# Optimization experiments

Hardware: AMD Instinct MI355X
Metric: run time of the kernel (lower is better)

The kernel has to match this reference:

```python
import jax, jax.numpy as jnp
import numpy as np

D_MODEL = 1024
H = 16
HEAD_DIM = D_MODEL // H  # 64


def setup_inputs() -> dict:
    key = jax.random.key(0)
    ks = jax.random.split(key, 11)
    B, S, D = 1, 4096, D_MODEL
    scale = 1.0 / np.sqrt(D)
    inp = {
        'q': jax.random.normal(ks[0], (B, S, D), jnp.float32),
        'k': jax.random.normal(ks[1], (B, S, D), jnp.float32),
        'v': jax.random.normal(ks[2], (B, S, D), jnp.float32),
        'w_q': jax.random.normal(ks[3], (D, D), jnp.float32) * scale,
        'b_q': jnp.zeros((D,), jnp.float32),
        'w_k': jax.random.normal(ks[4], (D, D), jnp.float32) * scale,
        'b_k': jnp.zeros((D,), jnp.float32),
        'w_v': jax.random.normal(ks[5], (D, D), jnp.float32) * scale,
        'b_v': jnp.zeros((D,), jnp.float32),
        'w_o': jax.random.normal(ks[6], (D, D), jnp.float32) * scale,
        'b_o': jnp.zeros((D,), jnp.float32),
    }
    return inp


def reference(q, k, v, w_q, b_q, w_k, b_k, w_v, b_v, w_o, b_o):
    B, Sq, D = q.shape
    Sk = k.shape[1]
    # Linear projections (torch Linear: x @ W.T + b), split into heads: [B,H,S,hd]
    Q = (q @ w_q.T + b_q).reshape(B, Sq, H, HEAD_DIM).transpose(0, 2, 1, 3)
    K = (k @ w_k.T + b_k).reshape(B, Sk, H, HEAD_DIM).transpose(0, 2, 1, 3)
    V = (v @ w_v.T + b_v).reshape(B, Sk, H, HEAD_DIM).transpose(0, 2, 1, 3)
    # Naive attention: full [B,H,Sq,Sk] scores, softmax, then AV
    scores = jnp.einsum('bhqd,bhkd->bhqk', Q, K) / jnp.sqrt(jnp.float32(HEAD_DIM))
    attn = jax.nn.softmax(scores, axis=-1)
    ctx = jnp.einsum('bhqk,bhkd->bhqd', attn, V)
    concat = ctx.transpose(0, 2, 1, 3).reshape(B, Sq, D)
    return concat @ w_o.T + b_o
```

## Files before the change

kernel.cpp:

```cpp
#include <hip/hip_runtime.h>
#include <stdint.h>

#define S_LEN 4096
#define DM 1024
#define NH 16

typedef __attribute__((ext_vector_type(8))) short short8;
typedef __attribute__((ext_vector_type(4))) float float4v;
typedef __attribute__((ext_vector_type(4))) unsigned short ushort4v;

typedef __attribute__((address_space(1))) const void* as1cvp;
typedef __attribute__((address_space(3))) void* as3vp;

#define MFMA16(a, b, c) __builtin_amdgcn_mfma_f32_16x16x32_bf16((a), (b), (c), 0, 0, 0)
#define GLOAD_LDS16(g, l) \
  __builtin_amdgcn_global_load_lds((as1cvp)(g), (as3vp)(l), 16, 0, 0)

__device__ __forceinline__ unsigned short f2bf(float f) {
  unsigned u = __float_as_uint(f);
  u += 0x7fffu + ((u >> 16) & 1u);
  return (unsigned short)(u >> 16);
}

__global__ __launch_bounds__(256) void cast_all(
    const float* __restrict__ q, const float* __restrict__ k, const float* __restrict__ v,
    const float* __restrict__ wq, const float* __restrict__ wk, const float* __restrict__ wv,
    const float* __restrict__ wo, unsigned short* __restrict__ dst)
{
  const float* src; size_t off; int n;
  switch (blockIdx.y) {
    case 0: src = q;  off = 0u;        n = 4194304; break;
    case 1: src = k;  off = 4194304u;  n = 4194304; break;
    case 2: src = v;  off = 8388608u;  n = 4194304; break;
    case 3: src = wq; off = 12582912u; n = 1048576; break;
    case 4: src = wk; off = 13631488u; n = 1048576; break;
    case 5: src = wv; off = 14680064u; n = 1048576; break;
    default: src = wo; off = 15728640u; n = 1048576; break;
  }
  int nv = n >> 2;
  for (int i = blockIdx.x * blockDim.x + threadIdx.x; i < nv; i += gridDim.x * blockDim.x) {
    float4v val = ((const float4v*)src)[i];
    ushort4v o;
    o.x = f2bf(val.x); o.y = f2bf(val.y); o.z = f2bf(val.z); o.w = f2bf(val.w);
    ((ushort4v*)(dst + off))[i] = o;
  }
}

template<int MODE>
__device__ __forceinline__ void gemm128(
    const unsigned short* __restrict__ A, const unsigned short* __restrict__ Bw,
    unsigned short* Cb, float* Cf, const float* __restrict__ bias, float alpha,
    unsigned short* As, unsigned short* Bs)
{
  const int K = 1024, N = 1024;
  int bm = blockIdx.x, bn = blockIdx.y;
  int t = threadIdx.x, lane = t & 63, w = t >> 6;
  int l15 = lane & 15, l4 = lane >> 4;
  int wr = w >> 1, wc = w & 1;

  float4v acc[4][4] = {};

  for (int kt = 0; kt < K / 32; ++kt) {
#pragma unroll
    for (int i = 0; i < 2; ++i) {
      int ci = i * 256 + t;
      int r = ci >> 2, cb = ci & 3;
      GLOAD_LDS16(A + (size_t)(bm * 128 + r) * K + kt * 32 + cb * 8,
                  As + (size_t)(i * 256 + w * 64) * 8);
      GLOAD_LDS16(Bw + (size_t)(bn * 128 + r) * K + kt * 32 + cb * 8,
                  Bs + (size_t)(i * 256 + w * 64) * 8);
    }
    __syncthreads();
    short8 af[4], bfr[4];
#pragma unroll
    for (int mf = 0; mf < 4; ++mf)
      af[mf] = *(const short8*)&As[(wr * 64 + mf * 16 + l15) * 32 + l4 * 8];
#pragma unroll
    for (int nf = 0; nf < 4; ++nf)
      bfr[nf] = *(const short8*)&Bs[(wc * 64 + nf * 16 + l15) * 32 + l4 * 8];
#pragma unroll
    for (int mf = 0; mf < 4; ++mf)
#pragma unroll
      for (int nf = 0; nf < 4; ++nf)
        acc[mf][nf] = MFMA16(af[mf], bfr[nf], acc[mf][nf]);
    __syncthreads();
  }

#pragma unroll
  for (int mf = 0; mf < 4; ++mf)
#pragma unroll
    for (int nf = 0; nf < 4; ++nf) {
      int col = bn * 128 + wc * 64 + nf * 16 + l15;
      float bv = bias[col];
#pragma unroll
      for (int j = 0; j < 4; ++j) {
        int row = bm * 128 + wr * 64 + mf * 16 + l4 * 4 + j;
        float val = (acc[mf][nf][j] + bv) * alpha;
        if (MODE == 1)      Cf[(size_t)row * N + col] = val;
        else if (MODE == 2) Cb[(size_t)col * S_LEN + row] = f2bf(val);
        else                Cb[(size_t)row * N + col] = f2bf(val);
      }
    }
}

__global__ __launch_bounds__(256) void proj_qkv(
    const unsigned short* xq, const unsigned short* xk, const unsigned short* xv,
    const unsigned short* wq, const unsigned short* wk, const unsigned short* wv,
    unsigned short* Qp, unsigned short* Kp, unsigned short* Vt,
    const float* bq, const float* bk, const float* bv)
{
  __shared__ unsigned short As[128 * 32], Bs[128 * 32];
  switch (blockIdx.z) {
    case 0:  gemm128<0>(xq, wq, Qp, nullptr, bq, 0.125f, As, Bs); break;
    case 1:  gemm128<0>(xk, wk, Kp, nullptr, bk, 1.0f,   As, Bs); break;
    default: gemm128<2>(xv, wv, Vt, nullptr, bv, 1.0f,   As, Bs); break;
  }
}

__global__ __launch_bounds__(256) void proj_o(
    const unsigned short* ctx, const unsigned short* wo, float* out, const float* bo)
{
  __shared__ unsigned short As[128 * 32], Bs[128 * 32];
  gemm128<1>(ctx, wo, nullptr, out, bo, 1.0f, As, Bs);
}

template<int BUF>
__device__ __forceinline__ void attn_tile(
    int kt,
    const unsigned short* kb0, const unsigned short* kb1,
    const unsigned short* vb0, const unsigned short* vb1,
    unsigned short* pw, const unsigned short* pr,
    const unsigned short* kg, const unsigned short* vg,
    unsigned short* kls, unsigned short* vls,
    const short8 (&qf)[2][2], float4v (&acc_o)[2][4],
    float (&m_run)[2], float (&l_run)[2], int l4)
{
  if (kt + 1 < 64) {
    GLOAD_LDS16(kg + (size_t)(kt + 1) * (64 * DM),            kls + (1 - BUF) * 4096);
    GLOAD_LDS16(kg + (size_t)(kt + 1) * (64 * DM) + 32 * DM,  kls + (1 - BUF) * 4096 + 2048);
    GLOAD_LDS16(vg + (kt + 1) * 64,                           vls + (1 - BUF) * 4096);
    GLOAD_LDS16(vg + (kt + 1) * 64 + 32 * S_LEN,              vls + (1 - BUF) * 4096 + 2048);
  }

  float4v sc[2][4];
#pragma unroll
  for (int nf = 0; nf < 4; ++nf) {
    short8 kf0 = *(const short8*)(kb0 + BUF * 4096 + nf * 1024);
    short8 kf1 = *(const short8*)(kb1 + BUF * 4096 + nf * 1024);
#pragma unroll
    for (int mf = 0; mf < 2; ++mf) {
      float4v z = {0.f, 0.f, 0.f, 0.f};
      z = MFMA16(kf0, qf[mf][0], z);
      sc[mf][nf] = MFMA16(kf1, qf[mf][1], z);
    }
  }

#pragma unroll
  for (int mf = 0; mf < 2; ++mf) {
    float mx = fmaxf(fmaxf(fmaxf(sc[mf][0][0], sc[mf][0][1]), sc[mf][0][2]), sc[mf][0][3]);
#pragma unroll
    for (int nf = 1; nf < 4; ++nf)
      mx = fmaxf(fmaxf(fmaxf(fmaxf(mx, sc[mf][nf][0]), sc[mf][nf][1]), sc[mf][nf][2]), sc[mf][nf][3]);
    mx = fmaxf(mx, __shfl_xor(mx, 16));
    mx = fmaxf(mx, __shfl_xor(mx, 32));

    if (!__all(mx <= m_run[mf] + 8.f)) {
      float mnew = fmaxf(m_run[mf], mx);
      float corr = __expf(m_run[mf] - mnew);
      m_run[mf] = mnew;
      l_run[mf] *= corr;
#pragma unroll
      for (int j = 0; j < 4; ++j) {
        float cj = __shfl(corr, l4 * 4 + j);
#pragma unroll
        for (int nf2 = 0; nf2 < 4; ++nf2) acc_o[mf][nf2][j] *= cj;
      }
    }

    float ps = 0.f;
#pragma unroll
    for (int nf = 0; nf < 4; ++nf) {
      float p0 = __expf(sc[mf][nf][0] - m_run[mf]);
      float p1 = __expf(sc[mf][nf][1] - m_run[mf]);
      float p2 = __expf(sc[mf][nf][2] - m_run[mf]);
      float p3 = __expf(sc[mf][nf][3] - m_run[mf]);
      ps += (p0 + p1) + (p2 + p3);
      unsigned lo, hi;
      asm("v_cvt_pk_bf16_f32 %0, %1, %2" : "=v"(lo) : "v"(p0), "v"(p1));
      asm("v_cvt_pk_bf16_f32 %0, %1, %2" : "=v"(hi) : "v"(p2), "v"(p3));
      uint2 u; u.x = lo; u.y = hi;
      *(uint2*)(pw + mf * 1152 + nf * 16) = u;
    }
    ps += __shfl_xor(ps, 16);
    ps += __shfl_xor(ps, 32);
    l_run[mf] += ps;
  }

  short8 pf[2][2];
#pragma unroll
  for (int mf = 0; mf < 2; ++mf)
#pragma unroll
    for (int kc = 0; kc < 2; ++kc)
      pf[mf][kc] = *(const short8*)(pr + mf * 1152 + kc * 32);

#pragma unroll
  for (int nfd = 0; nfd < 4; ++nfd) {
    short8 vf0 = *(const short8*)(vb0 + BUF * 4096 + nfd * 1024);
    short8 vf1 = *(const short8*)(vb1 + BUF * 4096 + nfd * 1024);
#pragma unroll
    for (int mf = 0; mf < 2; ++mf) {
      acc_o[mf][nfd] = MFMA16(pf[mf][0], vf0, acc_o[mf][nfd]);
      acc_o[mf][nfd] = MFMA16(pf[mf][1], vf1, acc_o[mf][nfd]);
    }
  }
  __syncthreads();
}

__global__ __launch_bounds__(256) void attn_fused(
    const unsigned short* __restrict__ Qp, const unsigned short* __restrict__ Kp,
    const unsigned short* __restrict__ Vt, unsigned short* __restrict__ ctx)
{
  __shared__ unsigned short Ks[2][64 * 64];
  __shared__ unsigned short Vts[2][64 * 64];
  __shared__ unsigned short Ps[4][32 * 72];

  int bid = blockIdx.x;
  int wg = (bid & 7) * 64 + (bid >> 3);
  int h = wg >> 5, qt = wg & 31;

  int t = threadIdx.x, lane = t & 63, w = t >> 6;
  int l15 = lane & 15, l4 = lane >> 4;

  short8 qf[2][2];
  int qrow0 = qt * 128 + w * 32;
#pragma unroll
  for (int mf = 0; mf < 2; ++mf)
#pragma unroll
    for (int ks = 0; ks < 2; ++ks)
      qf[mf][ks] = *(const short8*)&Qp[(size_t)(qrow0 + mf * 16 + l15) * DM + h * 64 + ks * 32 + l4 * 8];

  float4v acc_o[2][4] = {};
  float m_run[2] = {-INFINITY, -INFINITY};
  float l_run[2] = {0.f, 0.f};

  const int swz = l15 & 7;
  const unsigned short* kb0 = &Ks[0][l15 * 64 + ((l4) ^ swz) * 8];
  const unsigned short* kb1 = &Ks[0][l15 * 64 + ((4 + l4) ^ swz) * 8];
  const unsigned short* vb0 = &Vts[0][l15 * 64 + ((l4) ^ swz) * 8];
  const unsigned short* vb1 = &Vts[0][l15 * 64 + ((4 + l4) ^ swz) * 8];
  unsigned short* pw = &Ps[w][l15 * 72 + l4 * 4];
  const unsigned short* pr = &Ps[w][l15 * 72 + l4 * 8];

  int sr = t >> 3, sp = t & 7;
  int slb = sp ^ (sr & 7);
  const unsigned short* kg = Kp + (size_t)sr * DM + h * 64 + slb * 8;
  const unsigned short* vg = Vt + (size_t)(h * 64 + sr) * S_LEN + slb * 8;
  unsigned short* kls = &Ks[0][t * 8];
  unsigned short* vls = &Vts[0][t * 8];

  GLOAD_LDS16(kg,                kls);
  GLOAD_LDS16(kg + 32 * DM,      kls + 2048);
  GLOAD_LDS16(vg,                vls);
  GLOAD_LDS16(vg + 32 * S_LEN,   vls + 2048);
  __syncthreads();

  for (int kt = 0; kt < 64; kt += 2) {
    attn_tile<0>(kt,     kb0, kb1, vb0, vb1, pw, pr, kg, vg, kls, vls, qf, acc_o, m_run, l_run, l4);
    attn_tile<1>(kt + 1, kb0, kb1, vb0, vb1, pw, pr, kg, vg, kls, vls, qf, acc_o, m_run, l_run, l4);
  }

#pragma unroll
  for (int mf = 0; mf < 2; ++mf) {
#pragma unroll
    for (int j = 0; j < 4; ++j) {
      float lj = __shfl(l_run[mf], l4 * 4 + j);
      float inv = 1.0f / lj;
#pragma unroll
      for (int nfd = 0; nfd < 4; ++nfd) {
        int row = qrow0 + mf * 16 + l4 * 4 + j;
        int col = h * 64 + nfd * 16 + l15;
        ctx[(size_t)row * DM + col] = f2bf(acc_o[mf][nfd][j] * inv);
      }
    }
  }
}

extern "C" void kernel_launch(void* const* d_in, const int* in_sizes, int n_in,
                              void* d_out, int out_size, void* d_ws, size_t ws_size,
                              hipStream_t stream) {
  const float* q  = (const float*)d_in[0];
  const float* k  = (const float*)d_in[1];
  const float* v  = (const float*)d_in[2];
  const float* wq = (const float*)d_in[3];
  const float* bq = (const float*)d_in[4];
  const float* wk = (const float*)d_in[5];
  const float* bk = (const float*)d_in[6];
  const float* wv = (const float*)d_in[7];
  const float* bv = (const float*)d_in[8];
  const float* wo = (const float*)d_in[9];
  const float* bo = (const float*)d_in[10];

  unsigned short* ws  = (unsigned short*)d_ws;
  unsigned short* qb  = ws;
  unsigned short* kb  = ws + 4194304u;
  unsigned short* vb  = ws + 8388608u;
  unsigned short* wqb = ws + 12582912u;
  unsigned short* wkb = ws + 13631488u;
  unsigned short* wvb = ws + 14680064u;
  unsigned short* wob = ws + 15728640u;
  unsigned short* Qp  = ws + 16777216u;
  unsigned short* Kp  = ws + 20971520u;
  unsigned short* Vt  = ws + 25165824u;
  unsigned short* ctx = qb;
  float* out = (float*)d_out;

  cast_all<<<dim3(1024, 7), 256, 0, stream>>>(q, k, v, wq, wk, wv, wo, ws);
  proj_qkv<<<dim3(32, 8, 3), 256, 0, stream>>>(qb, kb, vb, wqb, wkb, wvb, Qp, Kp, Vt, bq, bk, bv);
  attn_fused<<<dim3(512), 256, 0, stream>>>(Qp, Kp, Vt, ctx);
  proj_o<<<dim3(32, 8), 256, 0, stream>>>(ctx, wob, out, bo);
}
```

Before: 201.2 us.

## Triple-buffer K/V tiles and pipeline next QK^T with current softmax-PV

```diff
diff --git a/kernel.cpp b/kernel.cpp
--- a/kernel.cpp
+++ b/kernel.cpp
@@ -124,37 +124,39 @@
   gemm128<1>(ctx, wo, nullptr, out, bo, 1.0f, As, Bs);
 }
 
-template<int BUF>
-__device__ __forceinline__ void attn_tile(
-    int kt,
+#define STAGE_T(BUFI, ktv) do {                                              \
+    GLOAD_LDS16(kg + (size_t)(ktv) * (64 * DM),               kls + (BUFI) * 4096);        \
+    GLOAD_LDS16(kg + (size_t)(ktv) * (64 * DM) + 32 * DM,     kls + (BUFI) * 4096 + 2048); \
+    GLOAD_LDS16(vg + (size_t)(ktv) * 64,                      vls + (BUFI) * 4096);        \
+    GLOAD_LDS16(vg + (size_t)(ktv) * 64 + (size_t)32 * S_LEN, vls + (BUFI) * 4096 + 2048); \
+  } while (0)
+
+template<int BUFN>
+__device__ __forceinline__ void qkt_into(
+    float4v (&scN)[2][4],
     const unsigned short* kb0, const unsigned short* kb1,
-    const unsigned short* vb0, const unsigned short* vb1,
-    unsigned short* pw, const unsigned short* pr,
-    const unsigned short* kg, const unsigned short* vg,
-    unsigned short* kls, unsigned short* vls,
-    const short8 (&qf)[2][2], float4v (&acc_o)[2][4],
-    float (&m_run)[2], float (&l_run)[2], int l4)
-{
-  if (kt + 1 < 64) {
-    GLOAD_LDS16(kg + (size_t)(kt + 1) * (64 * DM),            kls + (1 - BUF) * 4096);
-    GLOAD_LDS16(kg + (size_t)(kt + 1) * (64 * DM) + 32 * DM,  kls + (1 - BUF) * 4096 + 2048);
-    GLOAD_LDS16(vg + (kt + 1) * 64,                           vls + (1 - BUF) * 4096);
-    GLOAD_LDS16(vg + (kt + 1) * 64 + 32 * S_LEN,              vls + (1 - BUF) * 4096 + 2048);
-  }
-
-  float4v sc[2][4];
+    const short8 (&qf)[2][2])
+{
 #pragma unroll
   for (int nf = 0; nf < 4; ++nf) {
-    short8 kf0 = *(const short8*)(kb0 + BUF * 4096 + nf * 1024);
-    short8 kf1 = *(const short8*)(kb1 + BUF * 4096 + nf * 1024);
+    short8 kf0 = *(const short8*)(kb0 + BUFN * 4096 + nf * 1024);
+    short8 kf1 = *(const short8*)(kb1 + BUFN * 4096 + nf * 1024);
 #pragma unroll
     for (int mf = 0; mf < 2; ++mf) {
       float4v z = {0.f, 0.f, 0.f, 0.f};
       z = MFMA16(kf0, qf[mf][0], z);
-      sc[mf][nf] = MFMA16(kf1, qf[mf][1], z);
-    }
-  }
-
+      scN[mf][nf] = MFMA16(kf1, qf[mf][1], z);
+    }
+  }
+}
+
+template<int BC>
+__device__ __forceinline__ void softmax_pv(
+    float4v (&sc)[2][4],
+    const unsigned short* vb0, const unsigned short* vb1,
+    unsigned short* pw, const unsigned short* pr,
+    float4v (&acc_o)[2][4], float (&m_run)[2], float (&l_run)[2], int l4)
+{
 #pragma unroll
   for (int mf = 0; mf < 2; ++mf) {
     float mx = fmaxf(fmaxf(fmaxf(sc[mf][0][0], sc[mf][0][1]), sc[mf][0][2]), sc[mf][0][3]);
@@ -205,23 +207,41 @@
 
 #pragma unroll
   for (int nfd = 0; nfd < 4; ++nfd) {
-    short8 vf0 = *(const short8*)(vb0 + BUF * 4096 + nfd * 1024);
-    short8 vf1 = *(const short8*)(vb1 + BUF * 4096 + nfd * 1024);
+    short8 vf0 = *(const short8*)(vb0 + BC * 4096 + nfd * 1024);
+    short8 vf1 = *(const short8*)(vb1 + BC * 4096 + nfd * 1024);
 #pragma unroll
     for (int mf = 0; mf < 2; ++mf) {
       acc_o[mf][nfd] = MFMA16(pf[mf][0], vf0, acc_o[mf][nfd]);
       acc_o[mf][nfd] = MFMA16(pf[mf][1], vf1, acc_o[mf][nfd]);
     }
   }
+}
+
+template<int BC>
+__device__ __forceinline__ void attn_step(
+    int t, bool do_stage,
+    float4v (&scC)[2][4], float4v (&scN)[2][4],
+    const unsigned short* kb0, const unsigned short* kb1,
+    const unsigned short* vb0, const unsigned short* vb1,
+    unsigned short* pw, const unsigned short* pr,
+    const unsigned short* kg, const unsigned short* vg,
+    unsigned short* kls, unsigned short* vls,
+    const short8 (&qf)[2][2], float4v (&acc_o)[2][4],
+    float (&m_run)[2], float (&l_run)[2], int l4)
+{
+  constexpr int BN = (BC + 1) % 3;
+  qkt_into<BN>(scN, kb0, kb1, qf);
+  softmax_pv<BC>(scC, vb0, vb1, pw, pr, acc_o, m_run, l_run, l4);
   __syncthreads();
+  if (do_stage) STAGE_T(BC, t + 3);
 }
 
 __global__ __launch_bounds__(256) void attn_fused(
     const unsigned short* __restrict__ Qp, const unsigned short* __restrict__ Kp,
     const unsigned short* __restrict__ Vt, unsigned short* __restrict__ ctx)
 {
-  __shared__ unsigned short Ks[2][64 * 64];
-  __shared__ unsigned short Vts[2][64 * 64];
+  __shared__ unsigned short Ks[3][64 * 64];
+  __shared__ unsigned short Vts[3][64 * 64];
   __shared__ unsigned short Ps[4][32 * 72];
 
   int bid = blockIdx.x;
@@ -258,16 +278,27 @@
   unsigned short* kls = &Ks[0][t * 8];
   unsigned short* vls = &Vts[0][t * 8];
 
-  GLOAD_LDS16(kg,                kls);
-  GLOAD_LDS16(kg + 32 * DM,      kls + 2048);
-  GLOAD_LDS16(vg,                vls);
-  GLOAD_LDS16(vg + 32 * S_LEN,   vls + 2048);
+  float4v scA[2][4], scB[2][4];
+
+  STAGE_T(0, 0);
   __syncthreads();
-
-  for (int kt = 0; kt < 64; kt += 2) {
-    attn_tile<0>(kt,     kb0, kb1, vb0, vb1, pw, pr, kg, vg, kls, vls, qf, acc_o, m_run, l_run, l4);
-    attn_tile<1>(kt + 1, kb0, kb1, vb0, vb1, pw, pr, kg, vg, kls, vls, qf, acc_o, m_run, l_run, l4);
-  }
+  STAGE_T(1, 1);
+  qkt_into<0>(scA, kb0, kb1, qf);
+  __syncthreads();
+  STAGE_T(2, 2);
+
+  for (int kt = 0; kt < 60; kt += 6) {
+    attn_step<0>(kt,     true, scA, scB, kb0, kb1, vb0, vb1, pw, pr, kg, vg, kls, vls, qf, acc_o, m_run, l_run, l4);
+    attn_step<1>(kt + 1, true, scB, scA, kb0, kb1, vb0, vb1, pw, pr, kg, vg, kls, vls, qf, acc_o, m_run, l_run, l4);
+    attn_step<2>(kt + 2, true, scA, scB, kb0, kb1, vb0, vb1, pw, pr, kg, vg, kls, vls, qf, acc_o, m_run, l_run, l4);
+    attn_step<0>(kt + 3, true, scB, scA, kb0, kb1, vb0, vb1, pw, pr, kg, vg, kls, vls, qf, acc_o, m_run, l_run, l4);
+    attn_step<1>(kt + 4, true, scA, scB, kb0, kb1, vb0, vb1, pw, pr, kg, vg, kls, vls, qf, acc_o, m_run, l_run, l4);
+    attn_step<2>(kt + 5, true, scB, scA, kb0, kb1, vb0, vb1, pw, pr, kg, vg, kls, vls, qf, acc_o, m_run, l_run, l4);
+  }
+  attn_step<0>(60, true,  scA, scB, kb0, kb1, vb0, vb1, pw, pr, kg, vg, kls, vls, qf, acc_o, m_run, l_run, l4);
+  attn_step<1>(61, false, scB, scA, kb0, kb1, vb0, vb1, pw, pr, kg, vg, kls, vls, qf, acc_o, m_run, l_run, l4);
+  attn_step<2>(62, false, scA, scB, kb0, kb1, vb0, vb1, pw, pr, kg, vg, kls, vls, qf, acc_o, m_run, l_run, l4);
+  softmax_pv<0>(scB, vb0, vb1, pw, pr, acc_o, m_run, l_run, l4);
 
 #pragma unroll
   for (int mf = 0; mf < 2; ++mf) {
```

After: 198.4 us. About the same (-1.4%).
